# Optimization experiments

Hardware: AMD Instinct MI355X
Metric: run time of the kernel (lower is better)

The kernel has to match this reference:

```python
import jax, jax.numpy as jnp
import numpy as np

HEADS = 16

def setup_inputs() -> dict:
    key = jax.random.key(0)
    ks = jax.random.split(key, 5)
    B, T, D = 4, 2048, 1024
    scale = 0.02
    return {
        "x": jax.random.normal(ks[0], (B, T, D), dtype=jnp.float32),
        "W_attn": jax.random.normal(ks[1], (D, 3 * D), dtype=jnp.float32) * scale,
        "b_attn": jax.random.normal(ks[2], (3 * D,), dtype=jnp.float32) * scale,
        "W_proj": jax.random.normal(ks[3], (D, D), dtype=jnp.float32) * scale,
        "b_proj": jax.random.normal(ks[4], (D,), dtype=jnp.float32) * scale,
    }

def reference(x, W_attn, b_attn, W_proj, b_proj):
    B, T, D = x.shape
    H = HEADS
    hd = D // H
    qkv = x @ W_attn + b_attn                      # [B, T, 3D]
    q, k, v = jnp.split(qkv, 3, axis=2)
    # [B, T, H, hd] -> [B, H, T, hd]
    q = q.reshape(B, T, H, hd).transpose(0, 2, 1, 3)
    k = k.reshape(B, T, H, hd).transpose(0, 2, 1, 3)
    v = v.reshape(B, T, H, hd).transpose(0, 2, 1, 3)
    scale = hd ** 0.5
    scores = jnp.einsum("bhqd,bhkd->bhqk", q, k) / scale
    causal = jnp.tril(jnp.ones((T, T), dtype=bool))
    scores = jnp.where(causal, scores, -jnp.inf)
    attn = jax.nn.softmax(scores, axis=-1)
    out = jnp.einsum("bhqk,bhkd->bhqd", attn, v)    # [B, H, T, hd]
    out = out.transpose(0, 2, 1, 3).reshape(B, T, D)
    return out @ W_proj + b_proj
```

## Files before the change

### kernel.cpp

```cpp
#include <hip/hip_runtime.h>
#include <hip/hip_bf16.h>

using bf16 = __hip_bfloat16;
typedef __attribute__((ext_vector_type(8))) __bf16 bf16x8;
typedef __attribute__((ext_vector_type(4))) float f32x4;

#define B_   4
#define T_   2048
#define D_   1024
#define H_   16
#define HD_  64
#define BH_  (B_ * H_)
#define BT_  (B_ * T_)

#define QSCALE 0.18033688011112042f

__device__ __forceinline__ void gld_lds16(const void* g, void* l) {
    __builtin_amdgcn_global_load_lds(
        (const __attribute__((address_space(1))) unsigned int*)g,
        (__attribute__((address_space(3))) unsigned int*)l,
        16, 0, 0);
}

__global__ void cast_kernel(const float* __restrict__ in, bf16* __restrict__ out, int n4) {
    int i = blockIdx.x * 256 + threadIdx.x;
    if (i >= n4) return;
    float4 v = reinterpret_cast<const float4*>(in)[i];
    union { bf16 h[4]; uint2 u; } tmp;
    tmp.h[0] = __float2bfloat16(v.x);
    tmp.h[1] = __float2bfloat16(v.y);
    tmp.h[2] = __float2bfloat16(v.z);
    tmp.h[3] = __float2bfloat16(v.w);
    reinterpret_cast<uint2*>(out)[i] = tmp.u;
}

__global__ void transpose_cast(const float* __restrict__ W, bf16* __restrict__ Wt,
                               int K, int N) {
    __shared__ float tile[32][33];
    int nb = blockIdx.x * 32, kb = blockIdx.y * 32;
    int tx = threadIdx.x, ty = threadIdx.y;
    #pragma unroll
    for (int i = 0; i < 32; i += 8)
        tile[ty + i][tx] = W[(size_t)(kb + ty + i) * N + nb + tx];
    __syncthreads();
    #pragma unroll
    for (int i = 0; i < 32; i += 8)
        Wt[(size_t)(nb + ty + i) * K + kb + tx] = __float2bfloat16(tile[tx][ty + i]);
}

template <int MODE>
__global__ __launch_bounds__(256)
void gemm_bt(const bf16* __restrict__ A, const bf16* __restrict__ Bt,
             const float* __restrict__ bias,
             bf16* __restrict__ Qo, bf16* __restrict__ Ko, bf16* __restrict__ Vo,
             float* __restrict__ Fo, int K) {
    const int bm = blockIdx.x * 128;
    const int bn = blockIdx.y * 128;
    const int tid  = threadIdx.x;
    const int wid  = tid >> 6;
    const int lane = tid & 63;
    const int wr = (wid >> 1) * 64;
    const int wc = (wid & 1) * 64;
    const int ln_g = lane >> 4;
    const int ln_c = lane & 15;

    __shared__ bf16 sm[2][2][128][32];

    f32x4 acc[4][4] = {};

    const int g_row0 = wid * 32 + (lane >> 2);
    const int g_chk  = ((lane & 3) ^ ((lane >> 3) & 3)) * 8;
    const int l_row0 = wid * 32;
    const int colx = (ln_g * 16) ^ (((ln_c >> 1) & 3) << 4);

#define STAGE(BUF_, K0_) {                                                              \
    gld_lds16(&A [(size_t)(bm + g_row0)      * K + (K0_) + g_chk], &sm[BUF_][0][l_row0][0]);      \
    gld_lds16(&A [(size_t)(bm + g_row0 + 16) * K + (K0_) + g_chk], &sm[BUF_][0][l_row0 + 16][0]); \
    gld_lds16(&Bt[(size_t)(bn + g_row0)      * K + (K0_) + g_chk], &sm[BUF_][1][l_row0][0]);      \
    gld_lds16(&Bt[(size_t)(bn + g_row0 + 16) * K + (K0_) + g_chk], &sm[BUF_][1][l_row0 + 16][0]); }

#define COMPUTE(BUF_) {                                                                  \
    bf16x8 af[4], bfr[4];                                                                \
    _Pragma("unroll")                                                                    \
    for (int m = 0; m < 4; ++m)                                                          \
        af[m] = *reinterpret_cast<const bf16x8*>(                                        \
            (const char*)&sm[BUF_][0][wr + m * 16 + ln_c][0] + colx);                    \
    _Pragma("unroll")                                                                    \
    for (int n = 0; n < 4; ++n)                                                          \
        bfr[n] = *reinterpret_cast<const bf16x8*>(                                       \
            (const char*)&sm[BUF_][1][wc + n * 16 + ln_c][0] + colx);                    \
    _Pragma("unroll")                                                                    \
    for (int m = 0; m < 4; ++m)                                                          \
        _Pragma("unroll")                                                                \
        for (int n = 0; n < 4; ++n)                                                      \
            acc[m][n] = __builtin_amdgcn_mfma_f32_16x16x32_bf16(af[m], bfr[n],           \
                                                                 acc[m][n], 0, 0, 0); }

    const int NT = K >> 5;
    STAGE(0, 0);
    __syncthreads();

    for (int t = 0; t < NT - 2; t += 2) {
        STAGE(1, (t + 1) * 32);
        COMPUTE(0);
        __syncthreads();
        STAGE(0, (t + 2) * 32);
        COMPUTE(1);
        __syncthreads();
    }
    STAGE(1, (NT - 1) * 32);
    COMPUTE(0);
    __syncthreads();
    COMPUTE(1);

#undef STAGE
#undef COMPUTE

    #pragma unroll
    for (int m = 0; m < 4; ++m) {
        #pragma unroll
        for (int n = 0; n < 4; ++n) {
            const int col = bn + wc + n * 16 + ln_c;
            const float bcol = bias[col];
            #pragma unroll
            for (int j = 0; j < 4; ++j) {
                const int row = bm + wr + m * 16 + ln_g * 4 + j;
                float v = acc[m][n][j] + bcol;
                if (MODE == 0) {
                    const int part = col >> 10;
                    const int cc = col & 1023;
                    const int h = cc >> 6, d = cc & 63;
                    const int b = row >> 11, t = row & 2047;
                    const int bh = b * H_ + h;
                    if (part == 0)
                        Qo[((size_t)bh * T_ + t) * HD_ + d] = __float2bfloat16(v * QSCALE);
                    else if (part == 1)
                        Ko[((size_t)bh * T_ + t) * HD_ + d] = __float2bfloat16(v);
                    else
                        Vo[((size_t)bh * HD_ + d) * T_ + t] = __float2bfloat16(v);
                } else {
                    Fo[(size_t)row * D_ + col] = v;
                }
            }
        }
    }
}

__global__ __launch_bounds__(256)
void attn_kernel(const bf16* __restrict__ Q, const bf16* __restrict__ K,
                 const bf16* __restrict__ Vt, bf16* __restrict__ ctx) {
    const int bh = blockIdx.x & 63;
    const int qt = 31 - (blockIdx.x >> 6);
    const int tid  = threadIdx.x;
    const int wave = tid >> 6;
    const int lane = tid & 63;
    const int ln_g = lane >> 4;
    const int ln_c = lane & 15;

    const bf16* Qp = Q  + (size_t)bh * T_ * HD_;
    const bf16* Kp = K  + (size_t)bh * T_ * HD_;
    const bf16* Vp = Vt + (size_t)bh * HD_ * T_;

    __shared__ bf16 Ks[64][72];
    __shared__ bf16 Vs[64][72];
    __shared__ bf16 Ps[4][16][72];

    const int srow = tid >> 3;
    const int sc8  = (tid & 7) * 8;

    const int b = bh >> 4, h = bh & 15;

    const int qbase = qt * 64;
    const int qglob = qbase + wave * 16 + ln_c;

    const bf16x8 qf0 = *reinterpret_cast<const bf16x8*>(&Qp[(size_t)qglob * HD_ + ln_g * 8]);
    const bf16x8 qf1 = *reinterpret_cast<const bf16x8*>(&Qp[(size_t)qglob * HD_ + 32 + ln_g * 8]);

    f32x4 o[4] = {};
    float m = -INFINITY, l = 0.f;

    const int nk = qt + 1;

    int4 kr0, kr1, vr0, vr1;
    kr0 = *reinterpret_cast<const int4*>(&Kp[(size_t)srow * HD_ + sc8]);
    kr1 = *reinterpret_cast<const int4*>(&Kp[(size_t)(srow + 32) * HD_ + sc8]);
    vr0 = *reinterpret_cast<const int4*>(&Vp[(size_t)srow * T_ + sc8]);
    vr1 = *reinterpret_cast<const int4*>(&Vp[(size_t)(srow + 32) * T_ + sc8]);
    *reinterpret_cast<int4*>(&Ks[srow][sc8])      = kr0;
    *reinterpret_cast<int4*>(&Ks[srow + 32][sc8]) = kr1;
    *reinterpret_cast<int4*>(&Vs[srow][sc8])      = vr0;
    *reinterpret_cast<int4*>(&Vs[srow + 32][sc8]) = vr1;
    __syncthreads();

    for (int it = 0; it < nk; ++it) {
        const int kb = it * 64;
        const bool notlast = (it + 1 < nk);
        if (notlast) {
            const int kn = kb + 64;
            kr0 = *reinterpret_cast<const int4*>(&Kp[(size_t)(kn + srow) * HD_ + sc8]);
            kr1 = *reinterpret_cast<const int4*>(&Kp[(size_t)(kn + srow + 32) * HD_ + sc8]);
            vr0 = *reinterpret_cast<const int4*>(&Vp[(size_t)srow * T_ + kn + sc8]);
            vr1 = *reinterpret_cast<const int4*>(&Vp[(size_t)(srow + 32) * T_ + kn + sc8]);
        }

        f32x4 st[4];
        __builtin_amdgcn_s_setprio(1);
        #pragma unroll
        for (int kk = 0; kk < 4; ++kk) {
            bf16x8 kfa = *reinterpret_cast<const bf16x8*>(&Ks[kk * 16 + ln_c][ln_g * 8]);
            bf16x8 kfb = *reinterpret_cast<const bf16x8*>(&Ks[kk * 16 + ln_c][32 + ln_g * 8]);
            f32x4 z = {0.f, 0.f, 0.f, 0.f};
            z = __builtin_amdgcn_mfma_f32_16x16x32_bf16(kfa, qf0, z, 0, 0, 0);
            z = __builtin_amdgcn_mfma_f32_16x16x32_bf16(kfb, qf1, z, 0, 0, 0);
            st[kk] = z;
        }
        __builtin_amdgcn_s_setprio(0);

        if (!notlast) {
            #pragma unroll
            for (int kk = 0; kk < 4; ++kk)
                #pragma unroll
                for (int j = 0; j < 4; ++j)
                    if (kb + kk * 16 + ln_g * 4 + j > qglob) st[kk][j] = -INFINITY;
        }

        float mx = -INFINITY;
        #pragma unroll
        for (int kk = 0; kk < 4; ++kk)
            #pragma unroll
            for (int j = 0; j < 4; ++j)
                mx = fmaxf(mx, st[kk][j]);
        mx = fmaxf(mx, __shfl_xor(mx, 16));
        mx = fmaxf(mx, __shfl_xor(mx, 32));
        if (!__all(mx - m <= 8.f)) {
            const float mnew = fmaxf(m, mx);
            const float alpha = exp2f(m - mnew);
            l *= alpha;
            #pragma unroll
            for (int dt = 0; dt < 4; ++dt)
                #pragma unroll
                for (int j = 0; j < 4; ++j)
                    o[dt][j] *= alpha;
            m = mnew;
        }
        float rs = 0.f;
        #pragma unroll
        for (int kk = 0; kk < 4; ++kk) {
            union { bf16 hh[4]; uint2 u; } pk;
            #pragma unroll
            for (int j = 0; j < 4; ++j) {
                float p = exp2f(st[kk][j] - m);
                rs += p;
                pk.hh[j] = __float2bfloat16(p);
            }
            *reinterpret_cast<uint2*>(&Ps[wave][ln_c][kk * 16 + ln_g * 4]) = pk.u;
        }
        rs += __shfl_xor(rs, 16);
        rs += __shfl_xor(rs, 32);
        l += rs;

        const bf16x8 pf0 = *reinterpret_cast<const bf16x8*>(&Ps[wave][ln_c][ln_g * 8]);
        const bf16x8 pf1 = *reinterpret_cast<const bf16x8*>(&Ps[wave][ln_c][32 + ln_g * 8]);
        __builtin_amdgcn_s_setprio(1);
        #pragma unroll
        for (int dt = 0; dt < 4; ++dt) {
            bf16x8 vfa = *reinterpret_cast<const bf16x8*>(&Vs[dt * 16 + ln_c][ln_g * 8]);
            bf16x8 vfb = *reinterpret_cast<const bf16x8*>(&Vs[dt * 16 + ln_c][32 + ln_g * 8]);
            o[dt] = __builtin_amdgcn_mfma_f32_16x16x32_bf16(vfa, pf0, o[dt], 0, 0, 0);
            o[dt] = __builtin_amdgcn_mfma_f32_16x16x32_bf16(vfb, pf1, o[dt], 0, 0, 0);
        }
        __builtin_amdgcn_s_setprio(0);

        if (notlast) {
            __syncthreads();
            *reinterpret_cast<int4*>(&Ks[srow][sc8])      = kr0;
            *reinterpret_cast<int4*>(&Ks[srow + 32][sc8]) = kr1;
            *reinterpret_cast<int4*>(&Vs[srow][sc8])      = vr0;
            *reinterpret_cast<int4*>(&Vs[srow + 32][sc8]) = vr1;
            __syncthreads();
        }
    }

    const float inv = 1.0f / l;
    bf16* dst = ctx + ((size_t)(b * T_ + qglob)) * D_ + h * HD_;
    #pragma unroll
    for (int dt = 0; dt < 4; ++dt) {
        union { bf16 hh[4]; uint2 u; } ok;
        #pragma unroll
        for (int j = 0; j < 4; ++j)
            ok.hh[j] = __float2bfloat16(o[dt][j] * inv);
        *reinterpret_cast<uint2*>(&dst[dt * 16 + ln_g * 4]) = ok.u;
    }
}

extern "C" void kernel_launch(void* const* d_in, const int* in_sizes, int n_in,
                              void* d_out, int out_size, void* d_ws, size_t ws_size,
                              hipStream_t stream) {
    const float* x      = (const float*)d_in[0];
    const float* W_attn = (const float*)d_in[1];
    const float* b_attn = (const float*)d_in[2];
    const float* W_proj = (const float*)d_in[3];
    const float* b_proj = (const float*)d_in[4];
    float* out = (float*)d_out;

    char* ws = (char*)d_ws;
    bf16* xh  = (bf16*)ws;  ws += (size_t)BT_ * D_ * 2;
    bf16* WaT = (bf16*)ws;  ws += (size_t)3 * D_ * D_ * 2;
    bf16* WpT = (bf16*)ws;  ws += (size_t)D_ * D_ * 2;
    bf16* Qb  = (bf16*)ws;  ws += (size_t)BH_ * T_ * HD_ * 2;
    bf16* Kb  = (bf16*)ws;  ws += (size_t)BH_ * T_ * HD_ * 2;
    bf16* Vb  = (bf16*)ws;  ws += (size_t)BH_ * T_ * HD_ * 2;
    bf16* ctx = (bf16*)ws;  ws += (size_t)BT_ * D_ * 2;

    cast_kernel<<<(BT_ * D_ / 4 + 255) / 256, 256, 0, stream>>>(x, xh, BT_ * D_ / 4);
    transpose_cast<<<dim3(3 * D_ / 32, D_ / 32), dim3(32, 8), 0, stream>>>(W_attn, WaT, D_, 3 * D_);
    transpose_cast<<<dim3(D_ / 32, D_ / 32), dim3(32, 8), 0, stream>>>(W_proj, WpT, D_, D_);

    gemm_bt<0><<<dim3(BT_ / 128, 3 * D_ / 128), 256, 0, stream>>>(
        xh, WaT, b_attn, Qb, Kb, Vb, nullptr, D_);

    attn_kernel<<<dim3(BH_ * 32), 256, 0, stream>>>(Qb, Kb, Vb, ctx);

    gemm_bt<1><<<dim3(BT_ / 128, D_ / 128), 256, 0, stream>>>(
        ctx, WpT, b_proj, nullptr, nullptr, nullptr, out, D_);
}
```

Measured before the change: 193.4 us.

## Feed P to PV MFMA from registers via 16x16x16 bf16, drop LDS staging

```diff
diff --git a/kernel.cpp b/kernel.cpp
--- a/kernel.cpp
+++ b/kernel.cpp
@@ -3,6 +3,7 @@
 
 using bf16 = __hip_bfloat16;
 typedef __attribute__((ext_vector_type(8))) __bf16 bf16x8;
+typedef __attribute__((ext_vector_type(4))) __bf16 bf16x4;
 typedef __attribute__((ext_vector_type(4))) float f32x4;
 
 #define B_   4
@@ -20,6 +21,22 @@
         (const __attribute__((address_space(1))) unsigned int*)g,
         (__attribute__((address_space(3))) unsigned int*)l,
         16, 0, 0);
+}
+
+__device__ __forceinline__ f32x4 mfma16(bf16x4 a, bf16x4 b, f32x4 c) {
+#if __has_builtin(__builtin_amdgcn_mfma_f32_16x16x16_bf16)
+    return __builtin_amdgcn_mfma_f32_16x16x16_bf16(a, b, c, 0, 0, 0);
+#elif __has_builtin(__builtin_amdgcn_mfma_f32_16x16x16bf16_1k)
+    typedef __attribute__((ext_vector_type(4))) short s16x4;
+    union U { bf16x4 h; s16x4 s; };
+    U ua, ub; ua.h = a; ub.h = b;
+    return __builtin_amdgcn_mfma_f32_16x16x16bf16_1k(ua.s, ub.s, c, 0, 0, 0);
+#else
+    f32x4 d;
+    asm volatile("v_mfma_f32_16x16x16_bf16 %0, %1, %2, %3\n\ts_nop 7\n\ts_nop 7"
+                 : "=v"(d) : "v"(a), "v"(b), "v"(c));
+    return d;
+#endif
 }
 
 __global__ void cast_kernel(const float* __restrict__ in, bf16* __restrict__ out, int n4) {
@@ -146,7 +163,7 @@
     }
 }
 
-__global__ __launch_bounds__(256)
+__global__ __launch_bounds__(256, 8)
 void attn_kernel(const bf16* __restrict__ Q, const bf16* __restrict__ K,
                  const bf16* __restrict__ Vt, bf16* __restrict__ ctx) {
     const int bh = blockIdx.x & 63;
@@ -163,7 +180,6 @@
 
     __shared__ bf16 Ks[64][72];
     __shared__ bf16 Vs[64][72];
-    __shared__ bf16 Ps[4][16][72];
 
     const int srow = tid >> 3;
     const int sc8  = (tid & 7) * 8;
@@ -230,10 +246,10 @@
             #pragma unroll
             for (int j = 0; j < 4; ++j)
                 mx = fmaxf(mx, st[kk][j]);
-        mx = fmaxf(mx, __shfl_xor(mx, 16));
-        mx = fmaxf(mx, __shfl_xor(mx, 32));
         if (!__all(mx - m <= 8.f)) {
-            const float mnew = fmaxf(m, mx);
+            float r = fmaxf(mx, __shfl_xor(mx, 16));
+            r = fmaxf(r, __shfl_xor(r, 32));
+            const float mnew = fmaxf(m, r);
             const float alpha = exp2f(m - mnew);
             l *= alpha;
             #pragma unroll
@@ -243,31 +259,27 @@
                     o[dt][j] *= alpha;
             m = mnew;
         }
-        float rs = 0.f;
+
+        union { bf16 hh[4]; bf16x4 v4; } pk[4];
         #pragma unroll
         for (int kk = 0; kk < 4; ++kk) {
-            union { bf16 hh[4]; uint2 u; } pk;
             #pragma unroll
             for (int j = 0; j < 4; ++j) {
                 float p = exp2f(st[kk][j] - m);
-                rs += p;
-                pk.hh[j] = __float2bfloat16(p);
+                l += p;
+                pk[kk].hh[j] = __float2bfloat16(p);
             }
-            *reinterpret_cast<uint2*>(&Ps[wave][ln_c][kk * 16 + ln_g * 4]) = pk.u;
-        }
-        rs += __shfl_xor(rs, 16);
-        rs += __shfl_xor(rs, 32);
-        l += rs;
-
-        const bf16x8 pf0 = *reinterpret_cast<const bf16x8*>(&Ps[wave][ln_c][ln_g * 8]);
-        const bf16x8 pf1 = *reinterpret_cast<const bf16x8*>(&Ps[wave][ln_c][32 + ln_g * 8]);
+        }
+
         __builtin_amdgcn_s_setprio(1);
         #pragma unroll
-        for (int dt = 0; dt < 4; ++dt) {
-            bf16x8 vfa = *reinterpret_cast<const bf16x8*>(&Vs[dt * 16 + ln_c][ln_g * 8]);
-            bf16x8 vfb = *reinterpret_cast<const bf16x8*>(&Vs[dt * 16 + ln_c][32 + ln_g * 8]);
-            o[dt] = __builtin_amdgcn_mfma_f32_16x16x32_bf16(vfa, pf0, o[dt], 0, 0, 0);
-            o[dt] = __builtin_amdgcn_mfma_f32_16x16x32_bf16(vfb, pf1, o[dt], 0, 0, 0);
+        for (int kk = 0; kk < 4; ++kk) {
+            #pragma unroll
+            for (int dt = 0; dt < 4; ++dt) {
+                bf16x4 vf = *reinterpret_cast<const bf16x4*>(
+                    &Vs[dt * 16 + ln_c][kk * 16 + ln_g * 4]);
+                o[dt] = mfma16(vf, pk[kk].v4, o[dt]);
+            }
         }
         __builtin_amdgcn_s_setprio(0);
 
@@ -281,6 +293,8 @@
         }
     }
 
+    l += __shfl_xor(l, 16);
+    l += __shfl_xor(l, 32);
     const float inv = 1.0f / l;
     bf16* dst = ctx + ((size_t)(b * T_ + qglob)) * D_ + h * HD_;
     #pragma unroll
```

After: 461.0 us. +138.4%, slower.
